# Kernel optimization log

Hardware: AMD Instinct MI355X
Metric: run time of the kernel (lower is better)

The kernel has to match this reference:

```python
import jax, jax.numpy as jnp
import numpy as np

B, S, NI = 8, 1024, 1024      # batch, seq_len, n_inputs
L, H, P = 128, 128, 64        # n_latents, hidden=n_inputs//8, prototype_dim
EPS_PROTO = 1e-4              # self.epsilon
BN_EPS = 1e-5                 # torch BatchNorm1d default eps


def setup_inputs() -> dict:
    key = jax.random.key(0)
    ks = jax.random.split(key, 4)
    return {
        "x": jax.random.normal(ks[0], (B, S, NI), jnp.float32),
        "W1": jax.random.normal(ks[1], (L, H, NI), jnp.float32) * 0.02,
        "b1": jnp.zeros((L, H), jnp.float32),
        "gamma": jnp.ones((L, H), jnp.float32),
        "beta": jnp.zeros((L, H), jnp.float32),
        "run_mean": jnp.zeros((L, H), jnp.float32),
        "run_var": jnp.ones((L, H), jnp.float32),
        "W2": jax.random.normal(ks[2], (L, P, H), jnp.float32) * 0.02,
        "b2": jnp.zeros((L, P), jnp.float32),
        "prototypes": jax.random.normal(ks[3], (L, P), jnp.float32) * 0.02,
    }


def reference(x, W1, b1, gamma, beta, run_mean, run_var, W2, b2, prototypes):
    Bb, Ss, _ = x.shape
    xf = x.reshape(Bb * Ss, NI)                       # [T, NI]
    # grouped first Linear over all latents at once: [T, L, H]
    h = jnp.einsum('ti,lhi->tlh', xf, W1) + b1
    # Dropout is identity in eval; BatchNorm1d in eval mode (running stats)
    h = (h - run_mean) * jax.lax.rsqrt(run_var + BN_EPS) * gamma + beta
    h = jax.nn.relu(h)
    # grouped second Linear: [T, L, P]
    enc = jnp.einsum('tlh,lph->tlp', h, W2) + b2
    # prototype L2-distance activation
    l2s = jnp.sum((enc - prototypes) ** 2, axis=-1)   # [T, L]
    raw = jnp.log((l2s + 1.0) / (l2s + EPS_PROTO))
    act = raw / jnp.log(1.0 / EPS_PROTO) * 300.0 - 100.0
    return act.reshape(Bb, Ss, L)
```

## Files before the change

### kernel.cpp

```cpp
#include <hip/hip_runtime.h>


#define NTOK 8192
#define NI   1024
#define NL   128
#define NH   128
#define NP   64

typedef __bf16 bf16x8 __attribute__((ext_vector_type(8)));
typedef float f32x4 __attribute__((ext_vector_type(4)));
typedef int   i32x4 __attribute__((ext_vector_type(4)));

static __device__ __forceinline__ unsigned short f2bf(float f) {
  union { float f; unsigned int u; } v; v.f = f;
  const unsigned int u = v.u;
  return (unsigned short)((u + 0x7fffu + ((u >> 16) & 1u)) >> 16);
}

__global__ void cvt_f32_bf16(const float* __restrict__ in,
                             unsigned short* __restrict__ out, int n8) {
  const int i = blockIdx.x * blockDim.x + threadIdx.x;
  if (i >= n8) return;
  const float4* p = (const float4*)in;
  const float4 a = p[2 * i], b = p[2 * i + 1];
  unsigned short v[8] __attribute__((aligned(16))) = {
      f2bf(a.x), f2bf(a.y), f2bf(a.z), f2bf(a.w),
      f2bf(b.x), f2bf(b.y), f2bf(b.z), f2bf(b.w)};
  ((uint4*)out)[i] = *(const uint4*)v;
}

__global__ void quant_rows_i8(const float* __restrict__ in,
                              signed char* __restrict__ outq,
                              float* __restrict__ scale, int nrows) {
  const int row = blockIdx.x * 4 + (threadIdx.x >> 6);
  if (row >= nrows) return;
  const int lane = threadIdx.x & 63;
  const float4* src = (const float4*)(in + (size_t)row * 1024);
  float4 v[4];
  float m = 0.f;
#pragma unroll
  for (int j = 0; j < 4; ++j) {
    v[j] = src[lane + 64 * j];
    m = fmaxf(m, fmaxf(fmaxf(fabsf(v[j].x), fabsf(v[j].y)),
                       fmaxf(fabsf(v[j].z), fabsf(v[j].w))));
  }
#pragma unroll
  for (int s = 1; s < 64; s <<= 1) m = fmaxf(m, __shfl_xor(m, s));
  m = fmaxf(m, 1e-20f);
  const float inv = 127.0f / m;
  if (lane == 0) scale[row] = m * (1.0f / 127.0f);
  unsigned int* dst = (unsigned int*)(outq + (size_t)row * 1024);
#pragma unroll
  for (int j = 0; j < 4; ++j) {
    const float qa = fminf(127.f, fmaxf(-127.f, v[j].x * inv));
    const float qb = fminf(127.f, fmaxf(-127.f, v[j].y * inv));
    const float qc = fminf(127.f, fmaxf(-127.f, v[j].z * inv));
    const float qd = fminf(127.f, fmaxf(-127.f, v[j].w * inv));
    const int a = (int)rintf(qa), b = (int)rintf(qb),
              c = (int)rintf(qc), d = (int)rintf(qd);
    dst[lane + 64 * j] = (unsigned)(a & 255) | ((unsigned)(b & 255) << 8) |
                         ((unsigned)(c & 255) << 16) | ((unsigned)(d & 255) << 24);
  }
}

static __device__ __forceinline__ void async16(const void* g, void* l) {
  __builtin_amdgcn_global_load_lds(
      (const __attribute__((address_space(1))) unsigned int*)g,
      (__attribute__((address_space(3))) unsigned int*)l, 16, 0, 0);
}

__global__ __launch_bounds__(256, 3) void proto_fused(
    const signed char* __restrict__ xq,
    const signed char* __restrict__ w1q,
    const unsigned short* __restrict__ w2b,
    const float* __restrict__ sx,
    const float* __restrict__ sw,
    const float* __restrict__ b1,
    const float* __restrict__ gamma, const float* __restrict__ beta,
    const float* __restrict__ rmean, const float* __restrict__ rvar,
    const float* __restrict__ b2,
    const float* __restrict__ protos,
    float* __restrict__ out)
{
  __shared__ __attribute__((aligned(128))) char smem[49152];
  const int tid  = threadIdx.x;
  const int wave = tid >> 6;
  const int lane = tid & 63;
  const int l15  = lane & 15;
  const int l4   = lane >> 4;
  const int wr   = wave >> 1;
  const int wc   = wave & 1;
  const int t0   = blockIdx.x * 128;
  const int lat  = blockIdx.y;

  const int srow  = lane >> 3;
  const int scolb = ((lane & 7) ^ srow) * 16;

  i32x4 acc[4][4] = {};

#pragma unroll
  for (int i = 0; i < 4; ++i) {
    const int r = wave * 4 + i * 16 + (lane >> 4);
    const int c = (lane & 15) ^ (r & 15);
    async16(w2b + (size_t)lat * NP * NH + r * NH + c * 8,
            smem + 32768 + (wave * 64 + i * 256) * 16);
  }

  auto stage = [&](int ks) {
    const int k0 = ks * 128;
#pragma unroll
    for (int j = 0; j < 4; ++j) {
      const int row = wave * 32 + j * 8 + srow;
      async16(xq + (size_t)(t0 + row) * NI + k0 + scolb,
              smem + (wave * 4 + j) * 1024);
      async16(w1q + (size_t)(lat * NH + row) * NI + k0 + scolb,
              smem + 16384 + (wave * 4 + j) * 1024);
    }
  };

  stage(0);
  const int rx = l15 & 7;
  for (int ks = 0; ks < 8; ++ks) {
    __syncthreads();
#pragma unroll
    for (int kk = 0; kk < 2; ++kk) {
      i32x4 a[4], b[4];
#pragma unroll
      for (int m = 0; m < 4; ++m)
        a[m] = *(const i32x4*)(smem + (wr * 64 + m * 16 + l15) * 128 +
                               (((kk * 4 + l4) ^ rx) << 4));
#pragma unroll
      for (int n = 0; n < 4; ++n)
        b[n] = *(const i32x4*)(smem + 16384 + (wc * 64 + n * 16 + l15) * 128 +
                               (((kk * 4 + l4) ^ rx) << 4));
#pragma unroll
      for (int m = 0; m < 4; ++m)
#pragma unroll
        for (int n = 0; n < 4; ++n)
          acc[m][n] = __builtin_amdgcn_mfma_i32_16x16x64_i8(a[m], b[n], acc[m][n], 0, 0, 0);
    }
    __syncthreads();
    if (ks + 1 < 8) stage(ks + 1);
  }

  float sxv[4][4];
#pragma unroll
  for (int m = 0; m < 4; ++m)
#pragma unroll
    for (int r = 0; r < 4; ++r)
      sxv[m][r] = sx[t0 + wr * 64 + m * 16 + l4 * 4 + r];

#pragma unroll
  for (int n = 0; n < 4; ++n) {
    const int hc = wc * 64 + n * 16 + l15;
    const int gi = lat * NH + hc;
    const float swc = sw[gi];
    const float sc  = gamma[gi] * rsqrtf(rvar[gi] + 1e-5f);
    const float bi  = beta[gi] - rmean[gi] * sc;
    const float bb  = b1[gi];
#pragma unroll
    for (int m = 0; m < 4; ++m)
#pragma unroll
      for (int r = 0; r < 4; ++r) {
        const float hv = (float)acc[m][n][r] * sxv[m][r] * swc;
        float v = (hv + bb) * sc + bi;
        v = v > 0.f ? v : 0.f;
        const int row = wr * 64 + m * 16 + l4 * 4 + r;
        const int pbyte = row * 256 + (((hc >> 3) ^ (row & 15)) << 4) + (hc & 7) * 2;
        *(unsigned short*)(smem + pbyte) = f2bf(v);
      }
  }
  __syncthreads();

  f32x4 acc2[2][4] = {};
#pragma unroll
  for (int kk = 0; kk < 4; ++kk) {
    const int pcsel = kk * 4 + l4;
    bf16x8 a2[2], bw[4];
#pragma unroll
    for (int m = 0; m < 2; ++m) {
      const int row = wave * 32 + m * 16 + l15;
      a2[m] = *(const bf16x8*)(smem + row * 256 + ((pcsel ^ (row & 15)) << 4));
    }
#pragma unroll
    for (int n = 0; n < 4; ++n) {
      const int rp = n * 16 + l15;
      bw[n] = *(const bf16x8*)(smem + 32768 + rp * 256 + ((pcsel ^ (rp & 15)) << 4));
    }
#pragma unroll
    for (int m = 0; m < 2; ++m)
#pragma unroll
      for (int n = 0; n < 4; ++n)
        acc2[m][n] = __builtin_amdgcn_mfma_f32_16x16x32_bf16(a2[m], bw[n], acc2[m][n], 0, 0, 0);
  }

  float pb[4], pp[4];
#pragma unroll
  for (int n = 0; n < 4; ++n) {
    const int p = n * 16 + l15;
    pb[n] = b2[lat * NP + p];
    pp[n] = protos[lat * NP + p];
  }
  const float act_scale = 300.0f / logf(10000.0f);
#pragma unroll
  for (int m = 0; m < 2; ++m)
#pragma unroll
    for (int r = 0; r < 4; ++r) {
      float s = 0.f;
#pragma unroll
      for (int n = 0; n < 4; ++n) {
        const float e = acc2[m][n][r] + pb[n] - pp[n];
        s += e * e;
      }
      s += __shfl_xor(s, 1);
      s += __shfl_xor(s, 2);
      s += __shfl_xor(s, 4);
      s += __shfl_xor(s, 8);
      if (l15 == 0) {
        const float a = logf((s + 1.0f) / (s + 1e-4f)) * act_scale - 100.0f;
        const int trow = wave * 32 + m * 16 + l4 * 4 + r;
        out[(size_t)(t0 + trow) * NL + lat] = a;
      }
    }
}

extern "C" void kernel_launch(void* const* d_in, const int* in_sizes, int n_in,
                              void* d_out, int out_size, void* d_ws, size_t ws_size,
                              hipStream_t stream) {
  const float* x      = (const float*)d_in[0];
  const float* W1     = (const float*)d_in[1];
  const float* b1     = (const float*)d_in[2];
  const float* gamma  = (const float*)d_in[3];
  const float* beta   = (const float*)d_in[4];
  const float* rmean  = (const float*)d_in[5];
  const float* rvar   = (const float*)d_in[6];
  const float* W2     = (const float*)d_in[7];
  const float* b2     = (const float*)d_in[8];
  const float* protos = (const float*)d_in[9];
  float* out = (float*)d_out;

  char* ws = (char*)d_ws;
  signed char*    xq  = (signed char*)ws;
  signed char*    w1q = (signed char*)(ws + (size_t)8 * 1024 * 1024);
  unsigned short* w2b = (unsigned short*)(ws + (size_t)24 * 1024 * 1024);
  float*          sx  = (float*)(ws + (size_t)26 * 1024 * 1024);
  float*          sw  = (float*)(ws + (size_t)26 * 1024 * 1024 + 64 * 1024);

  quant_rows_i8<<<NTOK / 4, 256, 0, stream>>>(x, xq, sx, NTOK);
  quant_rows_i8<<<NL * NH / 4, 256, 0, stream>>>(W1, w1q, sw, NL * NH);
  {
    const int n8w2 = NL * NP * NH / 8;
    cvt_f32_bf16<<<(n8w2 + 255) / 256, 256, 0, stream>>>(W2, w2b, n8w2);
  }

  dim3 grid(NTOK / 128, NL);
  proto_fused<<<grid, 256, 0, stream>>>(xq, w1q, w2b, sx, sw, b1, gamma, beta,
                                        rmean, rvar, b2, protos, out);
}
```

Measured before the change: 229.2 us.

## Merge quantization launches and simplify fused epilogue arithmetic

Replaces the two int8 row-quantization launches for x and W1 with one combined launch that picks its source by row index, which removes one kernel launch and its tail. It also folds the dequant scale, bias and batch-norm affine into a single FMA per element and uses the hardware bf16 conversion for the hidden tile. The final log of a ratio becomes a difference of two fast log2 calls scaled by ln2. These are small savings in the epilogue; the fast log2 may change rounding slightly.

```diff
diff --git a/kernel.cpp b/kernel.cpp
--- a/kernel.cpp
+++ b/kernel.cpp
@@ -29,18 +29,33 @@
   ((uint4*)out)[i] = *(const uint4*)v;
 }
 
-__global__ void quant_rows_i8(const float* __restrict__ in,
-                              signed char* __restrict__ outq,
-                              float* __restrict__ scale, int nrows) {
+__global__ void quant_rows_i8_dual(const float* __restrict__ x,
+                                   const float* __restrict__ w1,
+                                   signed char* __restrict__ xq,
+                                   signed char* __restrict__ w1q,
+                                   float* __restrict__ sx,
+                                   float* __restrict__ sw) {
   const int row = blockIdx.x * 4 + (threadIdx.x >> 6);
-  if (row >= nrows) return;
   const int lane = threadIdx.x & 63;
-  const float4* src = (const float4*)(in + (size_t)row * 1024);
+  const float* src;
+  unsigned int* dst;
+  float* sp;
+  if (row < NTOK) {
+    src = x + (size_t)row * 1024;
+    dst = (unsigned int*)(xq + (size_t)row * 1024);
+    sp  = sx + row;
+  } else {
+    const int r = row - NTOK;
+    src = w1 + (size_t)r * 1024;
+    dst = (unsigned int*)(w1q + (size_t)r * 1024);
+    sp  = sw + r;
+  }
+  const float4* s4 = (const float4*)src;
   float4 v[4];
   float m = 0.f;
 #pragma unroll
   for (int j = 0; j < 4; ++j) {
-    v[j] = src[lane + 64 * j];
+    v[j] = s4[lane + 64 * j];
     m = fmaxf(m, fmaxf(fmaxf(fabsf(v[j].x), fabsf(v[j].y)),
                        fmaxf(fabsf(v[j].z), fabsf(v[j].w))));
   }
@@ -48,16 +63,13 @@
   for (int s = 1; s < 64; s <<= 1) m = fmaxf(m, __shfl_xor(m, s));
   m = fmaxf(m, 1e-20f);
   const float inv = 127.0f / m;
-  if (lane == 0) scale[row] = m * (1.0f / 127.0f);
-  unsigned int* dst = (unsigned int*)(outq + (size_t)row * 1024);
+  if (lane == 0) *sp = m * (1.0f / 127.0f);
 #pragma unroll
   for (int j = 0; j < 4; ++j) {
-    const float qa = fminf(127.f, fmaxf(-127.f, v[j].x * inv));
-    const float qb = fminf(127.f, fmaxf(-127.f, v[j].y * inv));
-    const float qc = fminf(127.f, fmaxf(-127.f, v[j].z * inv));
-    const float qd = fminf(127.f, fmaxf(-127.f, v[j].w * inv));
-    const int a = (int)rintf(qa), b = (int)rintf(qb),
-              c = (int)rintf(qc), d = (int)rintf(qd);
+    const int a = (int)rintf(fminf(127.f, fmaxf(-127.f, v[j].x * inv)));
+    const int b = (int)rintf(fminf(127.f, fmaxf(-127.f, v[j].y * inv)));
+    const int c = (int)rintf(fminf(127.f, fmaxf(-127.f, v[j].z * inv)));
+    const int d = (int)rintf(fminf(127.f, fmaxf(-127.f, v[j].w * inv)));
     dst[lane + 64 * j] = (unsigned)(a & 255) | ((unsigned)(b & 255) << 8) |
                          ((unsigned)(c & 255) << 16) | ((unsigned)(d & 255) << 24);
   }
@@ -124,15 +136,14 @@
     __syncthreads();
 #pragma unroll
     for (int kk = 0; kk < 2; ++kk) {
+      const int koff = ((kk * 4 + l4) ^ rx) << 4;
       i32x4 a[4], b[4];
 #pragma unroll
       for (int m = 0; m < 4; ++m)
-        a[m] = *(const i32x4*)(smem + (wr * 64 + m * 16 + l15) * 128 +
-                               (((kk * 4 + l4) ^ rx) << 4));
+        a[m] = *(const i32x4*)(smem + (wr * 64 + m * 16 + l15) * 128 + koff);
 #pragma unroll
       for (int n = 0; n < 4; ++n)
-        b[n] = *(const i32x4*)(smem + 16384 + (wc * 64 + n * 16 + l15) * 128 +
-                               (((kk * 4 + l4) ^ rx) << 4));
+        b[n] = *(const i32x4*)(smem + 16384 + (wc * 64 + n * 16 + l15) * 128 + koff);
 #pragma unroll
       for (int m = 0; m < 4; ++m)
 #pragma unroll
@@ -154,20 +165,19 @@
   for (int n = 0; n < 4; ++n) {
     const int hc = wc * 64 + n * 16 + l15;
     const int gi = lat * NH + hc;
-    const float swc = sw[gi];
-    const float sc  = gamma[gi] * rsqrtf(rvar[gi] + 1e-5f);
-    const float bi  = beta[gi] - rmean[gi] * sc;
-    const float bb  = b1[gi];
+    const float sc_ = gamma[gi] * rsqrtf(rvar[gi] + 1e-5f);
+    const float Kc  = sw[gi] * sc_;
+    const float Cc  = b1[gi] * sc_ + beta[gi] - rmean[gi] * sc_;
+    const int cchunk = hc >> 3, cin = (hc & 7) * 2;
 #pragma unroll
     for (int m = 0; m < 4; ++m)
 #pragma unroll
       for (int r = 0; r < 4; ++r) {
-        const float hv = (float)acc[m][n][r] * sxv[m][r] * swc;
-        float v = (hv + bb) * sc + bi;
+        float v = fmaf((float)acc[m][n][r] * sxv[m][r], Kc, Cc);
         v = v > 0.f ? v : 0.f;
         const int row = wr * 64 + m * 16 + l4 * 4 + r;
-        const int pbyte = row * 256 + (((hc >> 3) ^ (row & 15)) << 4) + (hc & 7) * 2;
-        *(unsigned short*)(smem + pbyte) = f2bf(v);
+        const int pbyte = row * 256 + ((cchunk ^ (l4 * 4 + r)) << 4) + cin;
+        *(__bf16*)(smem + pbyte) = (__bf16)v;
       }
   }
   __syncthreads();
@@ -201,7 +211,7 @@
     pb[n] = b2[lat * NP + p];
     pp[n] = protos[lat * NP + p];
   }
-  const float act_scale = 300.0f / logf(10000.0f);
+  const float scale2 = 0.69314718056f * 300.0f / logf(10000.0f);
 #pragma unroll
   for (int m = 0; m < 2; ++m)
 #pragma unroll
@@ -217,7 +227,7 @@
       s += __shfl_xor(s, 4);
       s += __shfl_xor(s, 8);
       if (l15 == 0) {
-        const float a = logf((s + 1.0f) / (s + 1e-4f)) * act_scale - 100.0f;
+        const float a = (__log2f(s + 1.0f) - __log2f(s + 1e-4f)) * scale2 - 100.0f;
         const int trow = wave * 32 + m * 16 + l4 * 4 + r;
         out[(size_t)(t0 + trow) * NL + lat] = a;
       }
@@ -246,8 +256,7 @@
   float*          sx  = (float*)(ws + (size_t)26 * 1024 * 1024);
   float*          sw  = (float*)(ws + (size_t)26 * 1024 * 1024 + 64 * 1024);
 
-  quant_rows_i8<<<NTOK / 4, 256, 0, stream>>>(x, xq, sx, NTOK);
-  quant_rows_i8<<<NL * NH / 4, 256, 0, stream>>>(W1, w1q, sw, NL * NH);
+  quant_rows_i8_dual<<<(NTOK + NL * NH) / 4, 256, 0, stream>>>(x, W1, xq, w1q, sx, sw);
   {
     const int n8w2 = NL * NP * NH / 8;
     cvt_f32_bf16<<<(n8w2 + 255) / 256, 256, 0, stream>>>(W2, w2b, n8w2);
```

New measurement: 222.9 us. -2.8%, faster.
